# Optimization experiments

Measured on AMD Instinct MI355X. Metric: run time of the kernel, lower is better.

Reference implementation:

```python
import jax, jax.numpy as jnp
import numpy as np

EMBED, HEADS, LEVELS, POINTS, MLP = 256, 8, 3, 4, 4
SHAPES = [(60, 80), (30, 40), (15, 20)]  # (H, W) per level


def layer_norm(x, g, b):
    m = jnp.mean(x, -1, keepdims=True)
    v = jnp.mean((x - m) ** 2, -1, keepdims=True)
    return (x - m) * jax.lax.rsqrt(v + 1e-5) * g + b


def _bilinear(v, H, W, gx, gy):
    # v: [B,h,H*W,dh]; gx,gy: [B,h,Nq,P] absolute pixel coords (grid_sample align_corners=False, zero padding)
    x0 = jnp.floor(gx); y0 = jnp.floor(gy)
    wx = gx - x0; wy = gy - y0

    def g(xi, yi):
        valid = ((xi >= 0) & (xi < W) & (yi >= 0) & (yi < H)).astype(v.dtype)
        idx = jnp.clip(yi, 0, H - 1) * W + jnp.clip(xi, 0, W - 1)
        B, h, Nq, P = idx.shape
        out = jnp.take_along_axis(v, idx.reshape(B, h, Nq * P)[..., None], axis=2)
        return out.reshape(B, h, Nq, P, -1) * valid[..., None]

    x0i = x0.astype(jnp.int32); y0i = y0.astype(jnp.int32)
    return (g(x0i, y0i) * ((1 - wx) * (1 - wy))[..., None]
            + g(x0i + 1, y0i) * (wx * (1 - wy))[..., None]
            + g(x0i, y0i + 1) * ((1 - wx) * wy)[..., None]
            + g(x0i + 1, y0i + 1) * (wx * wy)[..., None])


def setup_inputs() -> dict:
    key = jax.random.key(0)
    ks = jax.random.split(key, 16)
    B, Nq, C = 2, 8192, EMBED
    Nv = sum(h * w for h, w in SHAPES)
    s = 0.02
    d = {
        'query': jax.random.normal(ks[0], (B, Nq, C), jnp.float32),
        'value': jax.random.normal(ks[1], (B, Nv, C), jnp.float32),
        'query_pos': jax.random.normal(ks[2], (B, Nq, C), jnp.float32),
        'ref_pts': jax.random.uniform(ks[3], (B, Nq, LEVELS, 2), jnp.float32),
        'spatial_shapes': jnp.array(SHAPES, jnp.int32),
        'level_start_index': jnp.array(np.cumsum([0] + [h * w for h, w in SHAPES[:-1]]), jnp.int32),
        'g1': jnp.ones((C,), jnp.float32), 'b1': jnp.zeros((C,), jnp.float32),
        'Wo': s * jax.random.normal(ks[4], (C, HEADS * LEVELS * POINTS * 2), jnp.float32),
        'bo': jnp.zeros((HEADS * LEVELS * POINTS * 2,), jnp.float32),
        'Wa': s * jax.random.normal(ks[5], (C, HEADS * LEVELS * POINTS), jnp.float32),
        'ba': jnp.zeros((HEADS * LEVELS * POINTS,), jnp.float32),
        'Wv': s * jax.random.normal(ks[6], (C, C), jnp.float32), 'bv': jnp.zeros((C,), jnp.float32),
        'Wp': s * jax.random.normal(ks[7], (C, C), jnp.float32), 'bp': jnp.zeros((C,), jnp.float32),
        'g2': jnp.ones((C,), jnp.float32), 'b2': jnp.zeros((C,), jnp.float32),
        'Wf1': s * jax.random.normal(ks[8], (C, MLP * C), jnp.float32), 'bf1': jnp.zeros((MLP * C,), jnp.float32),
        'Wf2': s * jax.random.normal(ks[9], (MLP * C, C), jnp.float32), 'bf2': jnp.zeros((C,), jnp.float32),
    }
    return d


def reference(query, value, query_pos, ref_pts, spatial_shapes, level_start_index,
              g1, b1, Wo, bo, Wa, ba, Wv, bv, Wp, bp, g2, b2, Wf1, bf1, Wf2, bf2):
    B, Nq, C = query.shape
    dh = C // HEADS
    shapes = np.asarray(spatial_shapes).tolist()
    starts = np.asarray(level_start_index).tolist()

    qn = layer_norm(query, g1, b1)           # pre-norm
    qa = qn + query_pos                       # positional embedding inside attn
    offs = (qa @ Wo + bo).reshape(B, Nq, HEADS, LEVELS, POINTS, 2)
    aw = jax.nn.softmax((qa @ Wa + ba).reshape(B, Nq, HEADS, LEVELS * POINTS), -1)
    aw = aw.reshape(B, Nq, HEADS, LEVELS, POINTS)
    v = (value @ Wv + bv).reshape(B, -1, HEADS, dh).transpose(0, 2, 1, 3)  # [B,h,Nv,dh]

    # offset_normalizer = (W, H) per level
    norm = jnp.array([[w, h] for h, w in shapes], jnp.float32)
    loc = ref_pts[:, :, None, :, None, :] + offs / norm[None, None, None, :, None, :]

    out = jnp.zeros((B, Nq, HEADS, dh), query.dtype)
    for l, (H, W) in enumerate(shapes):
        vl = jax.lax.dynamic_slice_in_dim(v, starts[l], H * W, axis=2)
        gl = loc[:, :, :, l].transpose(0, 2, 1, 3, 4)   # [B,h,Nq,P,2]
        gx = gl[..., 0] * W - 0.5
        gy = gl[..., 1] * H - 0.5
        sampled = _bilinear(vl, H, W, gx, gy)            # [B,h,Nq,P,dh]
        out = out + jnp.einsum('bhqpd,bqhp->bqhd', sampled, aw[:, :, :, l])

    attn = out.reshape(B, Nq, C) @ Wp + bp + qn          # output proj + mmcv internal residual (identity=norm1(query))
    q = query + attn                                     # layer residual
    q2 = layer_norm(q, g2, b2)
    return q + (jax.nn.gelu(q2 @ Wf1 + bf1, approximate=False) @ Wf2 + bf2)
```

## Files before the change

### kernel.cpp

```cpp
#include <hip/hip_runtime.h>
#include <math.h>


typedef short short8 __attribute__((ext_vector_type(8)));
typedef short s16x4 __attribute__((ext_vector_type(4)));
typedef __bf16 bf16x8 __attribute__((ext_vector_type(8)));
typedef float f32x4 __attribute__((ext_vector_type(4)));

__device__ __forceinline__ short f2b(float f) {
  unsigned u = __builtin_bit_cast(unsigned, f);
  u += 0x7fffu + ((u >> 16) & 1u);
  return (short)(u >> 16);
}
__device__ __forceinline__ float b2f(short s) {
  unsigned u = ((unsigned)(unsigned short)s) << 16;
  return __builtin_bit_cast(float, u);
}
__device__ __forceinline__ void b8f(short8 s, float* f) {
  const uint4 u = __builtin_bit_cast(uint4, s);
  f[0] = __builtin_bit_cast(float, u.x << 16);
  f[1] = __builtin_bit_cast(float, u.x & 0xffff0000u);
  f[2] = __builtin_bit_cast(float, u.y << 16);
  f[3] = __builtin_bit_cast(float, u.y & 0xffff0000u);
  f[4] = __builtin_bit_cast(float, u.z << 16);
  f[5] = __builtin_bit_cast(float, u.z & 0xffff0000u);
  f[6] = __builtin_bit_cast(float, u.w << 16);
  f[7] = __builtin_bit_cast(float, u.w & 0xffff0000u);
}

__device__ __forceinline__ f32x4 mfma16(short8 a, short8 b, f32x4 c) {
  return __builtin_amdgcn_mfma_f32_16x16x32_bf16(
      __builtin_bit_cast(bf16x8, a), __builtin_bit_cast(bf16x8, b), c, 0, 0, 0);
}

typedef __attribute__((address_space(3))) unsigned int lds_u32;
typedef const __attribute__((address_space(1))) unsigned int glb_u32;
__device__ __forceinline__ void glds16(const void* g, void* l) {
  __builtin_amdgcn_global_load_lds((glb_u32*)g, (lds_u32*)l, 16, 0, 0);
}

__device__ __forceinline__ float gelu1(float v) {
  return 0.5f * v * (1.f + erff(v * 0.70710678118654752f));
}

template <int EPI>
__device__ __forceinline__ void gemm64_core(
    int bx, int by,
    const short* __restrict__ A, const short* __restrict__ Bt,
    const float* __restrict__ bias, const float* __restrict__ bias2,
    void* __restrict__ Cout, int M, int Nreal, int ldc, int K, char* smem)
{
  short* sA = (short*)smem;
  short* sB = sA + 4096;
  float* sf = (float*)smem;

  const int t = threadIdx.x;
  const int wave = t >> 6, lane = t & 63;
  const int quad = lane >> 4, l16 = lane & 15;
  const int wm = (wave & 1) * 32, wn = (wave >> 1) * 64;
  const int m0 = by * 64, n0 = bx * 128;

  f32x4 acc[2][4];
#pragma unroll
  for (int i = 0; i < 2; i++)
#pragma unroll
    for (int j = 0; j < 4; j++) acc[i][j] = (f32x4){0.f, 0.f, 0.f, 0.f};

  const int srow = lane >> 3, pos = lane & 7;
  const int chunk = (pos + srow) & 7;
  const short* gA = A + (size_t)(m0 + wave * 16 + srow) * K + chunk * 8;
  const short* gB = Bt + (size_t)(n0 + wave * 32 + srow) * K + chunk * 8;

  const int nk = K >> 6;
  for (int kt = 0; kt < nk; ++kt) {
    if (kt) __syncthreads();
    const int ko = kt * 64;
#pragma unroll
    for (int g = 0; g < 2; ++g)
      glds16(gA + ko + (size_t)(g * 8) * K, sA + (wave * 16 + g * 8) * 64);
#pragma unroll
    for (int g = 0; g < 4; ++g)
      glds16(gB + ko + (size_t)(g * 8) * K, sB + (wave * 32 + g * 8) * 64);
    __syncthreads();
#pragma unroll
    for (int kk = 0; kk < 2; ++kk) {
      short8 af[2], bf[4];
      const int c = kk * 4 + quad;
#pragma unroll
      for (int i = 0; i < 2; i++) {
        const int lrA = wm + i * 16 + l16;
        af[i] = *(const short8*)&sA[lrA * 64 + ((c - lrA) & 7) * 8];
      }
#pragma unroll
      for (int j = 0; j < 4; j++) {
        const int lrB = wn + j * 16 + l16;
        bf[j] = *(const short8*)&sB[lrB * 64 + ((c - lrB) & 7) * 8];
      }
#pragma unroll
      for (int i = 0; i < 2; i++)
#pragma unroll
        for (int j = 0; j < 4; j++) acc[i][j] = mfma16(bf[j], af[i], acc[i][j]);
    }
  }
  __syncthreads();

#pragma unroll
  for (int b = 0; b < 2; ++b) {
    if (wm == b * 32) {
#pragma unroll
      for (int i = 0; i < 2; ++i) {
        const int rr = i * 16 + l16;
#pragma unroll
        for (int j = 0; j < 4; ++j)
          *(f32x4*)&sf[rr * 132 + wn + quad * 4 + j * 16] = acc[i][j];
      }
    }
    __syncthreads();
#pragma unroll
    for (int r2 = 0; r2 < 4; ++r2) {
      const int fidx = r2 * 1024 + t * 4;
      const int row = fidx >> 7, col = fidx & 127;
      const int gm = m0 + b * 32 + row;
      const int cc = n0 + col;
      if (gm < M && cc < Nreal) {
        const float4 v = *(const float4*)&sf[row * 132 + col];
        float4 bb;
        if (EPI == 4) bb = (cc < 192) ? *(const float4*)(bias + cc)
                                      : *(const float4*)(bias2 + cc - 192);
        else bb = *(const float4*)(bias + cc);
        float v0 = v.x + bb.x, v1 = v.y + bb.y, v2 = v.z + bb.z, v3 = v.w + bb.w;
        s16x4 o; o.x = f2b(v0); o.y = f2b(v1); o.z = f2b(v2); o.w = f2b(v3);
        *(s16x4*)((short*)Cout + (size_t)gm * ldc + cc) = o;
      }
    }
    __syncthreads();
  }
}

__global__ __launch_bounds__(256) void gemm_oa_v(
    const short* __restrict__ qa, const short* __restrict__ wt_oa,
    const float* __restrict__ bo, const float* __restrict__ ba,
    short* __restrict__ oabuf,
    const short* __restrict__ valbf, const short* __restrict__ wt_v,
    const float* __restrict__ bv, short* __restrict__ vproj)
{
  __shared__ __align__(16) char smem[24576];
  const int idx = blockIdx.x;
  if (idx < 768) {
    gemm64_core<4>(idx % 3, idx / 3, qa, wt_oa, bo, ba,
                   oabuf, 16384, 288, 288, 256, smem);
  } else {
    const int r = idx - 768;
    gemm64_core<5>(r % 2, r / 2, valbf, wt_v, bv, nullptr,
                   vproj, 12600, 256, 256, 256, smem);
  }
}

__global__ __launch_bounds__(1024, 4) void wp_mlp(
    const short* __restrict__ sampled,
    const short* __restrict__ wtp,
    const float* __restrict__ bp,
    const short* __restrict__ qnb,
    const float* __restrict__ query,
    const float* __restrict__ g2, const float* __restrict__ b2v,
    const short* __restrict__ wf1,
    const float* __restrict__ b1v,
    const short* __restrict__ wf2,
    const float* __restrict__ bf2v,
    float* __restrict__ outp)
{
  __shared__ __align__(16) char smem[163840];
  float* Q  = (float*)smem;
  short* H  = (short*)(smem + 65536);
  float* QY = (float*)(smem + 65536);
  short* RA = (short*)(smem + 131072);

  const int t = threadIdx.x;
  const int w = t >> 6, lane = t & 63;
  const int quad = lane >> 4, l16 = lane & 15;
  const int wm2 = w >> 3, wn8 = w & 7;
  const int m0 = blockIdx.x * 64;

#pragma unroll
  for (int q = 0; q < 2; ++q) {
    const int row = q * 32 + w * 2 + (lane >> 5);
    const int pos = lane & 31;
    const int cl = (pos & ~7) | ((pos + row) & 7);
    glds16(sampled + (size_t)(m0 + row) * 256 + cl * 8, RA + q * 8192 + w * 512);
  }
#pragma unroll
  for (int q = 0; q < 4; ++q) {
    const int row = q * 16 + w;
    glds16(query + (size_t)(m0 + row) * 256 + lane * 4, QY + row * 256);
  }
  __syncthreads();

  {
    f32x4 accp[2][2];
#pragma unroll
    for (int i = 0; i < 2; i++)
#pragma unroll
      for (int j = 0; j < 2; j++) accp[i][j] = (f32x4){0.f, 0.f, 0.f, 0.f};
#pragma unroll
    for (int kk = 0; kk < 8; ++kk) {
      const int c = kk * 4 + quad;
      short8 bfr[2], afr[2];
#pragma unroll
      for (int j = 0; j < 2; ++j) {
        const int n1 = wn8 * 2 + j;
        bfr[j] = *(const short8*)(wtp + ((size_t)n1 * 32 + c) * 128 + l16 * 8);
      }
#pragma unroll
      for (int i = 0; i < 2; ++i) {
        const int r = wm2 * 32 + i * 16 + l16;
        const int pos = (c & ~7) | ((c - r) & 7);
        afr[i] = *(const short8*)(RA + r * 256 + pos * 8);
      }
#pragma unroll
      for (int i = 0; i < 2; ++i)
#pragma unroll
        for (int j = 0; j < 2; ++j) accp[i][j] = mfma16(bfr[j], afr[i], accp[i][j]);
    }
#pragma unroll
    for (int i = 0; i < 2; ++i)
#pragma unroll
      for (int j = 0; j < 2; ++j) {
        const int r = wm2 * 32 + i * 16 + l16;
        const int c = wn8 * 32 + j * 16 + quad * 4;
        *(f32x4*)&Q[r * 256 + (c ^ ((r & 7) << 2))] = accp[i][j];
      }
  }
  __syncthreads();

  {
    const float4 bbp  = *(const float4*)(bp + lane * 4);
    const float4 gv   = *(const float4*)(g2 + lane * 4);
    const float4 bb2  = *(const float4*)(b2v + lane * 4);
#pragma unroll
    for (int rep = 0; rep < 4; ++rep) {
      const int row = rep * 16 + w;
      const int gm = m0 + row;
      const int cs = (lane * 4) ^ ((row & 7) << 2);
      const float4 a  = *(const float4*)&Q[row * 256 + cs];
      const float4 qv = *(const float4*)&QY[row * 256 + lane * 4];
      const s16x4 qn  = *(const s16x4*)(qnb + (size_t)gm * 256 + lane * 4);
      float v0 = a.x + bbp.x + b2f(qn.x) + qv.x;
      float v1 = a.y + bbp.y + b2f(qn.y) + qv.y;
      float v2 = a.z + bbp.z + b2f(qn.z) + qv.z;
      float v3 = a.w + bbp.w + b2f(qn.w) + qv.w;
      float s = v0 + v1 + v2 + v3;
#pragma unroll
      for (int o = 32; o; o >>= 1) s += __shfl_xor(s, o);
      const float mean = s * (1.f / 256.f);
      const float d0 = v0 - mean, d1 = v1 - mean, d2 = v2 - mean, d3 = v3 - mean;
      float ss = d0 * d0 + d1 * d1 + d2 * d2 + d3 * d3;
#pragma unroll
      for (int o = 32; o; o >>= 1) ss += __shfl_xor(ss, o);
      const float inv = rsqrtf(ss * (1.f / 256.f) + 1e-5f);
      *(f32x4*)&Q[row * 256 + cs] = (f32x4){v0, v1, v2, v3};
      const int col = lane * 4;
      const int c = col >> 3;
      const int pos = (c & ~7) | ((c - row) & 7);
      s16x4 o2;
      o2.x = f2b(d0 * inv * gv.x + bb2.x);
      o2.y = f2b(d1 * inv * gv.y + bb2.y);
      o2.z = f2b(d2 * inv * gv.z + bb2.z);
      o2.w = f2b(d3 * inv * gv.w + bb2.w);
      *(s16x4*)(RA + row * 256 + pos * 8 + (col & 7)) = o2;
    }
  }
  __syncthreads();

  f32x4 acc2[2][2];
#pragma unroll
  for (int i = 0; i < 2; i++)
#pragma unroll
    for (int j = 0; j < 2; j++) acc2[i][j] = (f32x4){0.f, 0.f, 0.f, 0.f};

  for (int h = 0; h < 2; ++h) {
    if (h) __syncthreads();
    f32x4 acc[4][2];
#pragma unroll
    for (int i = 0; i < 4; i++)
#pragma unroll
      for (int j = 0; j < 2; j++) acc[i][j] = (f32x4){0.f, 0.f, 0.f, 0.f};
#pragma unroll
    for (int kk = 0; kk < 8; ++kk) {
      const int cg = kk * 4 + quad;
      short8 bfr[2], afr[4];
#pragma unroll
      for (int j = 0; j < 2; ++j) {
        const int n1 = h * 32 + w * 2 + j;
        bfr[j] = *(const short8*)(wf1 + ((size_t)n1 * 32 + cg) * 128 + l16 * 8);
      }
#pragma unroll
      for (int i = 0; i < 4; ++i) {
        const int r = i * 16 + l16;
        const int pos = (cg & ~7) | ((cg - r) & 7);
        afr[i] = *(const short8*)(RA + r * 256 + pos * 8);
      }
#pragma unroll
      for (int i = 0; i < 4; ++i)
#pragma unroll
        for (int j = 0; j < 2; ++j) acc[i][j] = mfma16(bfr[j], afr[i], acc[i][j]);
    }
#pragma unroll
    for (int j = 0; j < 2; ++j) {
      const int coll = (w * 2 + j) * 16 + quad * 4;
      const float4 bb = *(const float4*)(b1v + h * 512 + coll);
      const int c = coll >> 3;
#pragma unroll
      for (int i = 0; i < 4; ++i) {
        const int r = i * 16 + l16;
        const int pos = (c & ~7) | ((c - r) & 7);
        s16x4 o;
        o.x = f2b(gelu1(acc[i][j].x + bb.x));
        o.y = f2b(gelu1(acc[i][j].y + bb.y));
        o.z = f2b(gelu1(acc[i][j].z + bb.z));
        o.w = f2b(gelu1(acc[i][j].w + bb.w));
        *(s16x4*)(H + r * 512 + pos * 8 + (coll & 7)) = o;
      }
    }
    __syncthreads();

#pragma unroll 4
    for (int kk = 0; kk < 16; ++kk) {
      const int cl = kk * 4 + quad;
      short8 bfr[2], afr[2];
#pragma unroll
      for (int j = 0; j < 2; ++j) {
        const int n1 = wn8 * 2 + j;
        bfr[j] = *(const short8*)(wf2 + ((size_t)n1 * 128 + h * 64 + cl) * 128 + l16 * 8);
      }
#pragma unroll
      for (int i = 0; i < 2; ++i) {
        const int r = wm2 * 32 + i * 16 + l16;
        const int pos = (cl & ~7) | ((cl - r) & 7);
        afr[i] = *(const short8*)(H + r * 512 + pos * 8);
      }
#pragma unroll
      for (int i = 0; i < 2; ++i)
#pragma unroll
        for (int j = 0; j < 2; ++j) acc2[i][j] = mfma16(bfr[j], afr[i], acc2[i][j]);
    }
  }
  __syncthreads();

#pragma unroll
  for (int i = 0; i < 2; ++i)
#pragma unroll
    for (int j = 0; j < 2; ++j) {
      const int r = wm2 * 32 + i * 16 + l16;
      const int c = wn8 * 32 + j * 16 + quad * 4;
      *(f32x4*)&QY[r * 256 + (c ^ ((r & 7) << 2))] = acc2[i][j];
    }
  __syncthreads();

  {
    const float4 bbf = *(const float4*)(bf2v + lane * 4);
#pragma unroll
    for (int rep = 0; rep < 4; ++rep) {
      const int row = rep * 16 + w;
      const int gm = m0 + row;
      const int cs = (lane * 4) ^ ((row & 7) << 2);
      const float4 v  = *(const float4*)&QY[row * 256 + cs];
      const float4 qb = *(const float4*)&Q[row * 256 + cs];
      *(float4*)(outp + (size_t)gm * 256 + lane * 4) =
          make_float4(v.x + bbf.x + qb.x, v.y + bbf.y + qb.y,
                      v.z + bbf.z + qb.z, v.w + bbf.w + qb.w);
    }
  }
}

__global__ __launch_bounds__(256) void prep_all(
    const float* __restrict__ Wo, const float* __restrict__ Wa,
    const float* __restrict__ Wv, const float* __restrict__ Wp,
    const float* __restrict__ Wf1, const float* __restrict__ Wf2,
    short* __restrict__ t_oa, short* __restrict__ t_v, short* __restrict__ t_p,
    short* __restrict__ t_f1, short* __restrict__ t_f2,
    const float* __restrict__ value, short* __restrict__ valbf,
    const float* __restrict__ query, const float* __restrict__ query_pos,
    const float* __restrict__ g1, const float* __restrict__ b1,
    short* __restrict__ qnb, short* __restrict__ qa)
{
  __shared__ float tile[32][33];
  const int t = threadIdx.x;
  const int blk = blockIdx.x;

  if (blk < 1792) {
    const int bxa = blk & 255, bya = blk >> 8;
    int K, N, noff; const float* src; short* dst;
    switch (bya) {
      case 0: src = Wo;      dst = t_oa; K = 256;  N = 192;  noff = 0;   break;
      case 1: src = Wa;      dst = t_oa; K = 256;  N = 96;   noff = 192; break;
      case 2: src = nullptr; dst = t_oa; K = 256;  N = 96;   noff = 288; break;
      case 3: src = Wv;      dst = t_v;  K = 256;  N = 256;  noff = 0;   break;
      case 4: src = Wp;      dst = t_p;  K = 256;  N = 256;  noff = 0;   break;
      case 5: src = Wf1;     dst = t_f1; K = 256;  N = 1024; noff = 0;   break;
      default: src = Wf2;    dst = t_f2; K = 1024; N = 256;  noff = 0;   break;
    }
    const bool fragpack = (bya >= 4);
    const int tilesK = K >> 5;
    const int nt = tilesK * (N >> 5);
    if (bxa >= nt) return;
    const int tk = bxa % tilesK, tn = bxa / tilesK;
    const int k0 = tk * 32, n0 = tn * 32;
    const int r = t >> 3, c4 = (t & 7) * 4;
    float4 v = make_float4(0.f, 0.f, 0.f, 0.f);
    if (src) v = *(const float4*)(src + (size_t)(k0 + r) * N + n0 + c4);
    tile[r][c4] = v.x; tile[r][c4 + 1] = v.y; tile[r][c4 + 2] = v.z; tile[r][c4 + 3] = v.w;
    __syncthreads();
    const int nn = t >> 3, kc = (t & 7) * 4;
    s16x4 o;
    o.x = f2b(tile[kc][nn]); o.y = f2b(tile[kc + 1][nn]);
    o.z = f2b(tile[kc + 2][nn]); o.w = f2b(tile[kc + 3][nn]);
    if (fragpack) {
      const int n = n0 + nn, k = k0 + kc;
      *(s16x4*)(dst + ((size_t)(n >> 4) * (K >> 3) + (k >> 3)) * 128 +
                (n & 15) * 8 + (k & 7)) = o;
    } else {
      *(s16x4*)(dst + (size_t)(noff + n0 + nn) * K + k0 + kc) = o;
    }
  } else if (blk < 1792 + 3169) {
    const int i = ((blk - 1792) * 256 + t) * 4;
    if (i >= 12672 * 256) return;
    s16x4 o = (s16x4){0, 0, 0, 0};
    if (i < 12600 * 256) {
      float4 v = *(const float4*)(value + i);
      o.x = f2b(v.x); o.y = f2b(v.y); o.z = f2b(v.z); o.w = f2b(v.w);
    }
    *(s16x4*)(valbf + i) = o;
  } else {
    const int row  = (blk - 4961) * 4 + (t >> 6);
    const int lane = t & 63;
    const float4 v = ((const float4*)(query + (size_t)row * 256))[lane];
    float s = v.x + v.y + v.z + v.w;
#pragma unroll
    for (int o = 32; o; o >>= 1) s += __shfl_xor(s, o);
    const float mean = s * (1.f / 256.f);
    const float dx = v.x - mean, dy = v.y - mean, dz = v.z - mean, dw = v.w - mean;
    float s2 = dx * dx + dy * dy + dz * dz + dw * dw;
#pragma unroll
    for (int o = 32; o; o >>= 1) s2 += __shfl_xor(s2, o);
    const float inv = rsqrtf(s2 * (1.f / 256.f) + 1e-5f);
    const float4 gv = ((const float4*)g1)[lane];
    const float4 bv = ((const float4*)b1)[lane];
    const float4 o1 = make_float4(dx * inv * gv.x + bv.x, dy * inv * gv.y + bv.y,
                                  dz * inv * gv.z + bv.z, dw * inv * gv.w + bv.w);
    s16x4 ob; ob.x = f2b(o1.x); ob.y = f2b(o1.y); ob.z = f2b(o1.z); ob.w = f2b(o1.w);
    ((s16x4*)(qnb + (size_t)row * 256))[lane] = ob;
    const float4 pv = ((const float4*)(query_pos + (size_t)row * 256))[lane];
    s16x4 op;
    op.x = f2b(o1.x + pv.x); op.y = f2b(o1.y + pv.y);
    op.z = f2b(o1.z + pv.z); op.w = f2b(o1.w + pv.w);
    ((s16x4*)(qa + (size_t)row * 256))[lane] = op;
  }
}

__global__ __launch_bounds__(256) void deform_fused(
    const short* __restrict__ vproj, const short* __restrict__ oa,
    const float* __restrict__ refp, short* __restrict__ out)
{
  __shared__ int4 sIdx[768];
  __shared__ s16x4 sW[768];
  const int t = threadIdx.x;

  if (t < 64) {
    const int row = blockIdx.x * 8 + (t >> 3), h = t & 7;
    const short* oarow = oa + (size_t)row * 288;
    float off[24];
    {
      const short8* op = (const short8*)(oarow + h * 24);
      b8f(op[0], off); b8f(op[1], off + 8); b8f(op[2], off + 16);
    }
    float lg[12];
    {
      const s16x4* ap = (const s16x4*)(oarow + 192 + h * 12);
#pragma unroll
      for (int i = 0; i < 3; i++) {
        const s16x4 v = ap[i];
        lg[i * 4] = b2f(v.x); lg[i * 4 + 1] = b2f(v.y);
        lg[i * 4 + 2] = b2f(v.z); lg[i * 4 + 3] = b2f(v.w);
      }
    }
    const float* rp = refp + (size_t)row * 6;
    const float Rx[3] = {rp[0], rp[2], rp[4]}, Ry[3] = {rp[1], rp[3], rp[5]};
    float mx = lg[0];
#pragma unroll
    for (int i = 1; i < 12; i++) mx = fmaxf(mx, lg[i]);
    float sum = 0.f;
#pragma unroll
    for (int i = 0; i < 12; i++) { lg[i] = __expf(lg[i] - mx); sum += lg[i]; }
    const float inv = 1.f / sum;
    const int b = row >> 13;
    const int Hs[3] = {60, 30, 15}, Ws[3] = {80, 40, 20}, St[3] = {0, 4800, 6000};
#pragma unroll
    for (int p = 0; p < 12; p++) {
      const int l = p >> 2;
      const int W = Ws[l], H = Hs[l];
      const float gx = Rx[l] * W + off[p * 2]     - 0.5f;
      const float gy = Ry[l] * H + off[p * 2 + 1] - 0.5f;
      const float x0f = floorf(gx), y0f = floorf(gy);
      const float wx = gx - x0f, wy = gy - y0f;
      const int x0 = (int)x0f, y0 = (int)y0f;
      const float aw = lg[p] * inv;
      float cw[4] = {(1.f - wx) * (1.f - wy), wx * (1.f - wy),
                     (1.f - wx) * wy, wx * wy};
      const int base = b * 6300 + St[l];
      int ci[4];
#pragma unroll
      for (int k = 0; k < 4; k++) {
        const int xx = x0 + (k & 1), yy = y0 + (k >> 1);
        const bool valid = (xx >= 0) & (xx < W) & (yy >= 0) & (yy < H);
        const int xc = min(max(xx, 0), W - 1);
        const int yc = min(max(yy, 0), H - 1);
        ci[k] = ((base + yc * W + xc) << 8) + h * 32;
        cw[k] = valid ? cw[k] * aw : 0.f;
      }
      sIdx[t * 12 + p] = make_int4(ci[0], ci[1], ci[2], ci[3]);
      s16x4 wv; wv.x = f2b(cw[0]); wv.y = f2b(cw[1]); wv.z = f2b(cw[2]); wv.w = f2b(cw[3]);
      sW[t * 12 + p] = wv;
    }
  }
  __syncthreads();

  const int lu = t >> 2, c4 = (t & 3) * 8;
  float acc[8];
#pragma unroll
  for (int i = 0; i < 8; i++) acc[i] = 0.f;
#pragma unroll 2
  for (int p = 0; p < 12; p++) {
    const int4 idx = sIdx[lu * 12 + p];
    const s16x4 wb = sW[lu * 12 + p];
    const float w0 = b2f(wb.x), w1 = b2f(wb.y), w2 = b2f(wb.z), w3 = b2f(wb.w);
    const short8 v0 = *(const short8*)(vproj + idx.x + c4);
    const short8 v1 = *(const short8*)(vproj + idx.y + c4);
    const short8 v2 = *(const short8*)(vproj + idx.z + c4);
    const short8 v3 = *(const short8*)(vproj + idx.w + c4);
    float f0[8], f1[8], f2[8], f3[8];
    b8f(v0, f0); b8f(v1, f1); b8f(v2, f2); b8f(v3, f3);
#pragma unroll
    for (int j = 0; j < 8; j++)
      acc[j] += w0 * f0[j] + w1 * f1[j] + w2 * f2[j] + w3 * f3[j];
  }
  short8 o;
#pragma unroll
  for (int j = 0; j < 8; j++) o[j] = f2b(acc[j]);
  *(short8*)(out + (size_t)(blockIdx.x * 256 + t) * 8) = o;
}

extern "C" void kernel_launch(void* const* d_in, const int* in_sizes, int n_in,
                              void* d_out, int out_size, void* d_ws, size_t ws_size,
                              hipStream_t stream)
{
  const float* query     = (const float*)d_in[0];
  const float* value     = (const float*)d_in[1];
  const float* query_pos = (const float*)d_in[2];
  const float* ref_pts   = (const float*)d_in[3];
  const float* g1  = (const float*)d_in[6];
  const float* b1  = (const float*)d_in[7];
  const float* Wo  = (const float*)d_in[8];
  const float* bo  = (const float*)d_in[9];
  const float* Wa  = (const float*)d_in[10];
  const float* ba  = (const float*)d_in[11];
  const float* Wv  = (const float*)d_in[12];
  const float* bv  = (const float*)d_in[13];
  const float* Wp  = (const float*)d_in[14];
  const float* bp  = (const float*)d_in[15];
  const float* g2  = (const float*)d_in[16];
  const float* b2  = (const float*)d_in[17];
  const float* Wf1 = (const float*)d_in[18];
  const float* bf1 = (const float*)d_in[19];
  const float* Wf2 = (const float*)d_in[20];
  const float* bf2 = (const float*)d_in[21];

  char* ws = (char*)d_ws;
  short* wt_oa   = (short*)(ws + 0);
  short* wt_v    = (short*)(ws + 196608);
  short* wt_p    = (short*)(ws + 327680);
  short* wt_f1   = (short*)(ws + 458752);
  short* wt_f2   = (short*)(ws + 983040);
  short* qnb     = (short*)(ws + 1507328);
  short* qa      = (short*)(ws + 18284544);
  short* oabuf   = (short*)(ws + 26673152);
  short* vproj   = (short*)(ws + 45547520);
  short* sampled = (short*)(ws + 51998720);
  short* valbf   = (short*)(ws + 77164544);
  float* outp = (float*)d_out;

  prep_all<<<9057, 256, 0, stream>>>(Wo, Wa, Wv, Wp, Wf1, Wf2,
                                     wt_oa, wt_v, wt_p, wt_f1, wt_f2,
                                     value, valbf, query, query_pos,
                                     g1, b1, qnb, qa);
  gemm_oa_v<<<1162, 256, 0, stream>>>(qa, wt_oa, bo, ba, oabuf,
                                      valbf, wt_v, bv, vproj);
  deform_fused<<<2048, 256, 0, stream>>>(vproj, oabuf, ref_pts, sampled);
  wp_mlp<<<256, 1024, 0, stream>>>(sampled, wt_p, bp, qnb, query, g2, b2,
                                   wt_f1, bf1, wt_f2, bf2, outp);
}
```

Measured before the change: 214.8 us.

## Shrink wp_mlp row tile to 32 rows with 512-thread blocks

The fused output-projection/MLP kernel now processes 32 rows per block with 8 waves instead of 64 rows with 16 waves. The grid doubles to 512 blocks and LDS per block halves, which spreads work across more CUs than the previous 256 blocks. Each wave now owns one 16-row slice and a wider column strip, reusing one A fragment across 4 to 8 B fragments. A VGPR cap of 128 is added via an attribute. The cost is that each weight fragment is fetched for half as many rows, so global weight traffic roughly doubles, and the register cap risks spills with 8 accumulators.

After: 248.8 us. +15.8%, slower.

```diff
diff --git a/kernel.cpp b/kernel.cpp
--- a/kernel.cpp
+++ b/kernel.cpp
@@ -6,6 +6,16 @@
 typedef short s16x4 __attribute__((ext_vector_type(4)));
 typedef __bf16 bf16x8 __attribute__((ext_vector_type(8)));
 typedef float f32x4 __attribute__((ext_vector_type(4)));
+
+#if defined(__has_attribute)
+#if __has_attribute(amdgpu_num_vgpr)
+#define WPMLP_REGS __attribute__((amdgpu_num_vgpr(128)))
+#else
+#define WPMLP_REGS
+#endif
+#else
+#define WPMLP_REGS
+#endif
 
 __device__ __forceinline__ short f2b(float f) {
   unsigned u = __builtin_bit_cast(unsigned, f);
@@ -156,7 +166,7 @@
   }
 }
 
-__global__ __launch_bounds__(1024, 4) void wp_mlp(
+__global__ __launch_bounds__(512) WPMLP_REGS void wp_mlp(
     const short* __restrict__ sampled,
     const short* __restrict__ wtp,
     const float* __restrict__ bp,
@@ -169,66 +179,59 @@
     const float* __restrict__ bf2v,
     float* __restrict__ outp)
 {
-  __shared__ __align__(16) char smem[163840];
+  __shared__ __align__(16) char smem[81920];
   float* Q  = (float*)smem;
-  short* H  = (short*)(smem + 65536);
-  float* QY = (float*)(smem + 65536);
-  short* RA = (short*)(smem + 131072);
+  short* H  = (short*)(smem + 32768);
+  float* QY = (float*)(smem + 32768);
+  short* RA = (short*)(smem + 65536);
 
   const int t = threadIdx.x;
   const int w = t >> 6, lane = t & 63;
   const int quad = lane >> 4, l16 = lane & 15;
-  const int wm2 = w >> 3, wn8 = w & 7;
-  const int m0 = blockIdx.x * 64;
+  const int wm2 = w >> 2, wn4 = w & 3;
+  const int m0 = blockIdx.x * 32;
 
 #pragma unroll
   for (int q = 0; q < 2; ++q) {
-    const int row = q * 32 + w * 2 + (lane >> 5);
-    const int pos = lane & 31;
-    const int cl = (pos & ~7) | ((pos + row) & 7);
-    glds16(sampled + (size_t)(m0 + row) * 256 + cl * 8, RA + q * 8192 + w * 512);
+    const int g = q * 512 + t;
+    const int row = g >> 5, p = g & 31;
+    const int cl = (p & ~7) | ((p + row) & 7);
+    glds16(sampled + (size_t)(m0 + row) * 256 + cl * 8,
+           RA + (q * 512 + w * 64) * 8);
   }
 #pragma unroll
   for (int q = 0; q < 4; ++q) {
-    const int row = q * 16 + w;
-    glds16(query + (size_t)(m0 + row) * 256 + lane * 4, QY + row * 256);
+    const int g = q * 512 + t;
+    glds16(query + (size_t)(m0 + (g >> 6)) * 256 + (g & 63) * 4,
+           QY + (q * 512 + w * 64) * 4);
   }
   __syncthreads();
 
   {
-    f32x4 accp[2][2];
-#pragma unroll
-    for (int i = 0; i < 2; i++)
-#pragma unroll
-      for (int j = 0; j < 2; j++) accp[i][j] = (f32x4){0.f, 0.f, 0.f, 0.f};
+    f32x4 accp[4];
+#pragma unroll
+    for (int j = 0; j < 4; j++) accp[j] = (f32x4){0.f, 0.f, 0.f, 0.f};
 #pragma unroll
     for (int kk = 0; kk < 8; ++kk) {
       const int c = kk * 4 + quad;
-      short8 bfr[2], afr[2];
-#pragma unroll
-      for (int j = 0; j < 2; ++j) {
-        const int n1 = wn8 * 2 + j;
+      const int r = wm2 * 16 + l16;
+      const int pos = (c & ~7) | ((c - r) & 7);
+      const short8 afr = *(const short8*)(RA + r * 256 + pos * 8);
+      short8 bfr[4];
+#pragma unroll
+      for (int j = 0; j < 4; ++j) {
+        const int n1 = wn4 * 4 + j;
         bfr[j] = *(const short8*)(wtp + ((size_t)n1 * 32 + c) * 128 + l16 * 8);
       }
 #pragma unroll
-      for (int i = 0; i < 2; ++i) {
-        const int r = wm2 * 32 + i * 16 + l16;
-        const int pos = (c & ~7) | ((c - r) & 7);
-        afr[i] = *(const short8*)(RA + r * 256 + pos * 8);
-      }
-#pragma unroll
-      for (int i = 0; i < 2; ++i)
-#pragma unroll
-        for (int j = 0; j < 2; ++j) accp[i][j] = mfma16(bfr[j], afr[i], accp[i][j]);
-    }
-#pragma unroll
-    for (int i = 0; i < 2; ++i)
-#pragma unroll
-      for (int j = 0; j < 2; ++j) {
-        const int r = wm2 * 32 + i * 16 + l16;
-        const int c = wn8 * 32 + j * 16 + quad * 4;
-        *(f32x4*)&Q[r * 256 + (c ^ ((r & 7) << 2))] = accp[i][j];
-      }
+      for (int j = 0; j < 4; ++j) accp[j] = mfma16(bfr[j], afr, accp[j]);
+    }
+#pragma unroll
+    for (int j = 0; j < 4; ++j) {
+      const int r = wm2 * 16 + l16;
+      const int c = wn4 * 64 + j * 16 + quad * 4;
+      *(f32x4*)&Q[r * 256 + (c ^ ((r & 7) << 2))] = accp[j];
+    }
   }
   __syncthreads();
 
@@ -238,7 +241,7 @@
     const float4 bb2  = *(const float4*)(b2v + lane * 4);
 #pragma unroll
     for (int rep = 0; rep < 4; ++rep) {
-      const int row = rep * 16 + w;
+      const int row = rep * 8 + w;
       const int gm = m0 + row;
       const int cs = (lane * 4) ^ ((row & 7) << 2);
       const float4 a  = *(const float4*)&Q[row * 256 + cs];
@@ -271,96 +274,77 @@
   }
   __syncthreads();
 
-  f32x4 acc2[2][2];
-#pragma unroll
-  for (int i = 0; i < 2; i++)
-#pragma unroll
-    for (int j = 0; j < 2; j++) acc2[i][j] = (f32x4){0.f, 0.f, 0.f, 0.f};
+  f32x4 acc2[4];
+#pragma unroll
+  for (int j = 0; j < 4; j++) acc2[j] = (f32x4){0.f, 0.f, 0.f, 0.f};
 
   for (int h = 0; h < 2; ++h) {
     if (h) __syncthreads();
-    f32x4 acc[4][2];
-#pragma unroll
-    for (int i = 0; i < 4; i++)
-#pragma unroll
-      for (int j = 0; j < 2; j++) acc[i][j] = (f32x4){0.f, 0.f, 0.f, 0.f};
+    f32x4 acc1[8];
+#pragma unroll
+    for (int j = 0; j < 8; j++) acc1[j] = (f32x4){0.f, 0.f, 0.f, 0.f};
 #pragma unroll
     for (int kk = 0; kk < 8; ++kk) {
       const int cg = kk * 4 + quad;
-      short8 bfr[2], afr[4];
-#pragma unroll
-      for (int j = 0; j < 2; ++j) {
-        const int n1 = h * 32 + w * 2 + j;
+      const int r = wm2 * 16 + l16;
+      const int pos = (cg & ~7) | ((cg - r) & 7);
+      const short8 afr = *(const short8*)(RA + r * 256 + pos * 8);
+      short8 bfr[8];
+#pragma unroll
+      for (int j = 0; j < 8; ++j) {
+        const int n1 = h * 32 + wn4 * 8 + j;
         bfr[j] = *(const short8*)(wf1 + ((size_t)n1 * 32 + cg) * 128 + l16 * 8);
       }
 #pragma unroll
-      for (int i = 0; i < 4; ++i) {
-        const int r = i * 16 + l16;
-        const int pos = (cg & ~7) | ((cg - r) & 7);
-        afr[i] = *(const short8*)(RA + r * 256 + pos * 8);
-      }
-#pragma unroll
-      for (int i = 0; i < 4; ++i)
-#pragma unroll
-        for (int j = 0; j < 2; ++j) acc[i][j] = mfma16(bfr[j], afr[i], acc[i][j]);
-    }
-#pragma unroll
-    for (int j = 0; j < 2; ++j) {
-      const int coll = (w * 2 + j) * 16 + quad * 4;
+      for (int j = 0; j < 8; ++j) acc1[j] = mfma16(bfr[j], afr, acc1[j]);
+    }
+#pragma unroll
+    for (int j = 0; j < 8; ++j) {
+      const int coll = wn4 * 128 + j * 16 + quad * 4;
       const float4 bb = *(const float4*)(b1v + h * 512 + coll);
       const int c = coll >> 3;
-#pragma unroll
-      for (int i = 0; i < 4; ++i) {
-        const int r = i * 16 + l16;
-        const int pos = (c & ~7) | ((c - r) & 7);
-        s16x4 o;
-        o.x = f2b(gelu1(acc[i][j].x + bb.x));
-        o.y = f2b(gelu1(acc[i][j].y + bb.y));
-        o.z = f2b(gelu1(acc[i][j].z + bb.z));
-        o.w = f2b(gelu1(acc[i][j].w + bb.w));
-        *(s16x4*)(H + r * 512 + pos * 8 + (coll & 7)) = o;
-      }
+      const int r = wm2 * 16 + l16;
+      const int pos = (c & ~7) | ((c - r) & 7);
+      s16x4 o;
+      o.x = f2b(gelu1(acc1[j].x + bb.x));
+      o.y = f2b(gelu1(acc1[j].y + bb.y));
+      o.z = f2b(gelu1(acc1[j].z + bb.z));
+      o.w = f2b(gelu1(acc1[j].w + bb.w));
+      *(s16x4*)(H + r * 512 + pos * 8 + (coll & 7)) = o;
     }
     __syncthreads();
 
 #pragma unroll 4
     for (int kk = 0; kk < 16; ++kk) {
       const int cl = kk * 4 + quad;
-      short8 bfr[2], afr[2];
-#pragma unroll
-      for (int j = 0; j < 2; ++j) {
-        const int n1 = wn8 * 2 + j;
+      const int r = wm2 * 16 + l16;
+      const int pos = (cl & ~7) | ((cl - r) & 7);
+      const short8 afr = *(const short8*)(H + r * 512 + pos * 8);
+      short8 bfr[4];
+#pragma unroll
+      for (int j = 0; j < 4; ++j) {
+        const int n1 = wn4 * 4 + j;
         bfr[j] = *(const short8*)(wf2 + ((size_t)n1 * 128 + h * 64 + cl) * 128 + l16 * 8);
       }
 #pragma unroll
-      for (int i = 0; i < 2; ++i) {
-        const int r = wm2 * 32 + i * 16 + l16;
-        const int pos = (cl & ~7) | ((cl - r) & 7);
-        afr[i] = *(const short8*)(H + r * 512 + pos * 8);
-      }
-#pragma unroll
-      for (int i = 0; i < 2; ++i)
-#pragma unroll
-        for (int j = 0; j < 2; ++j) acc2[i][j] = mfma16(bfr[j], afr[i], acc2[i][j]);
-    }
-  }
-  __syncthreads();
-
-#pragma unroll
-  for (int i = 0; i < 2; ++i)
-#pragma unroll
-    for (int j = 0; j < 2; ++j) {
-      const int r = wm2 * 32 + i * 16 + l16;
-      const int c = wn8 * 32 + j * 16 + quad * 4;
-      *(f32x4*)&QY[r * 256 + (c ^ ((r & 7) << 2))] = acc2[i][j];
-    }
+      for (int j = 0; j < 4; ++j) acc2[j] = mfma16(bfr[j], afr, acc2[j]);
+    }
+  }
+  __syncthreads();
+
+#pragma unroll
+  for (int j = 0; j < 4; ++j) {
+    const int r = wm2 * 16 + l16;
+    const int c = wn4 * 64 + j * 16 + quad * 4;
+    *(f32x4*)&QY[r * 256 + (c ^ ((r & 7) << 2))] = acc2[j];
+  }
   __syncthreads();
 
   {
     const float4 bbf = *(const float4*)(bf2v + lane * 4);
 #pragma unroll
     for (int rep = 0; rep < 4; ++rep) {
-      const int row = rep * 16 + w;
+      const int row = rep * 8 + w;
       const int gm = m0 + row;
       const int cs = (lane * 4) ^ ((row & 7) << 2);
       const float4 v  = *(const float4*)&QY[row * 256 + cs];
@@ -595,6 +579,6 @@
   gemm_oa_v<<<1162, 256, 0, stream>>>(qa, wt_oa, bo, ba, oabuf,
                                       valbf, wt_v, bv, vproj);
   deform_fused<<<2048, 256, 0, stream>>>(vproj, oabuf, ref_pts, sampled);
-  wp_mlp<<<256, 1024, 0, stream>>>(sampled, wt_p, bp, qnb, query, g2, b2,
-                                   wt_f1, bf1, wt_f2, bf2, outp);
-}
+  wp_mlp<<<512, 512, 0, stream>>>(sampled, wt_p, bp, qnb, query, g2, b2,
+                                  wt_f1, bf1, wt_f2, bf2, outp);
+}
```

## Restructure wp_mlp hidden loop into four 256-wide chunks and shrink LDS

Applied to the files above, without the earlier changes.

The fused projection+MLP kernel now processes the 1024-wide hidden layer in four 256-column chunks instead of two 512-wide halves. Both GEMMs use the same 2x8 wave tiling, which shrinks the H buffer and total LDS from 160KB to 128KB. The query residual is read directly from global memory instead of being staged in LDS, and the final bias+residual is fused into Q in registers before the store. The launch bound no longer requests a minimum of 4 waves per EU and caps VGPRs at 128. In exchange there are more block-wide barriers per row tile and the weight fragments are reloaded per chunk.

Result: faster. 206.9 us (-3.6%).

```diff
diff --git a/kernel.cpp b/kernel.cpp
--- a/kernel.cpp
+++ b/kernel.cpp
@@ -6,6 +6,16 @@
 typedef short s16x4 __attribute__((ext_vector_type(4)));
 typedef __bf16 bf16x8 __attribute__((ext_vector_type(8)));
 typedef float f32x4 __attribute__((ext_vector_type(4)));
+
+#if defined(__has_attribute)
+#if __has_attribute(amdgpu_num_vgpr)
+#define WPMLP_REGS __attribute__((amdgpu_num_vgpr(128)))
+#else
+#define WPMLP_REGS
+#endif
+#else
+#define WPMLP_REGS
+#endif
 
 __device__ __forceinline__ short f2b(float f) {
   unsigned u = __builtin_bit_cast(unsigned, f);
@@ -156,7 +166,7 @@
   }
 }
 
-__global__ __launch_bounds__(1024, 4) void wp_mlp(
+__global__ __launch_bounds__(1024) WPMLP_REGS void wp_mlp(
     const short* __restrict__ sampled,
     const short* __restrict__ wtp,
     const float* __restrict__ bp,
@@ -169,11 +179,10 @@
     const float* __restrict__ bf2v,
     float* __restrict__ outp)
 {
-  __shared__ __align__(16) char smem[163840];
+  __shared__ __align__(16) char smem[131072];
   float* Q  = (float*)smem;
   short* H  = (short*)(smem + 65536);
-  float* QY = (float*)(smem + 65536);
-  short* RA = (short*)(smem + 131072);
+  short* RA = (short*)(smem + 98304);
 
   const int t = threadIdx.x;
   const int w = t >> 6, lane = t & 63;
@@ -182,16 +191,12 @@
   const int m0 = blockIdx.x * 64;
 
 #pragma unroll
-  for (int q = 0; q < 2; ++q) {
-    const int row = q * 32 + w * 2 + (lane >> 5);
-    const int pos = lane & 31;
-    const int cl = (pos & ~7) | ((pos + row) & 7);
-    glds16(sampled + (size_t)(m0 + row) * 256 + cl * 8, RA + q * 8192 + w * 512);
-  }
-#pragma unroll
-  for (int q = 0; q < 4; ++q) {
-    const int row = q * 16 + w;
-    glds16(query + (size_t)(m0 + row) * 256 + lane * 4, QY + row * 256);
+  for (int qq = 0; qq < 2; ++qq) {
+    const int g = qq * 1024 + t;
+    const int row = g >> 5, p = g & 31;
+    const int cl = (p & ~7) | ((p + row) & 7);
+    glds16(sampled + (size_t)(m0 + row) * 256 + cl * 8,
+           RA + (qq * 1024 + w * 64) * 8);
   }
   __syncthreads();
 
@@ -204,12 +209,7 @@
 #pragma unroll
     for (int kk = 0; kk < 8; ++kk) {
       const int c = kk * 4 + quad;
-      short8 bfr[2], afr[2];
-#pragma unroll
-      for (int j = 0; j < 2; ++j) {
-        const int n1 = wn8 * 2 + j;
-        bfr[j] = *(const short8*)(wtp + ((size_t)n1 * 32 + c) * 128 + l16 * 8);
-      }
+      short8 afr[2], bfr[2];
 #pragma unroll
       for (int i = 0; i < 2; ++i) {
         const int r = wm2 * 32 + i * 16 + l16;
@@ -217,6 +217,11 @@
         afr[i] = *(const short8*)(RA + r * 256 + pos * 8);
       }
 #pragma unroll
+      for (int j = 0; j < 2; ++j) {
+        const int n1 = wn8 * 2 + j;
+        bfr[j] = *(const short8*)(wtp + ((size_t)n1 * 32 + c) * 128 + l16 * 8);
+      }
+#pragma unroll
       for (int i = 0; i < 2; ++i)
 #pragma unroll
         for (int j = 0; j < 2; ++j) accp[i][j] = mfma16(bfr[j], afr[i], accp[i][j]);
@@ -226,8 +231,8 @@
 #pragma unroll
       for (int j = 0; j < 2; ++j) {
         const int r = wm2 * 32 + i * 16 + l16;
-        const int c = wn8 * 32 + j * 16 + quad * 4;
-        *(f32x4*)&Q[r * 256 + (c ^ ((r & 7) << 2))] = accp[i][j];
+        const int cc = wn8 * 32 + j * 16 + quad * 4;
+        *(f32x4*)&Q[r * 256 + (cc ^ ((r & 7) << 2))] = accp[i][j];
       }
   }
   __syncthreads();
@@ -242,7 +247,7 @@
       const int gm = m0 + row;
       const int cs = (lane * 4) ^ ((row & 7) << 2);
       const float4 a  = *(const float4*)&Q[row * 256 + cs];
-      const float4 qv = *(const float4*)&QY[row * 256 + lane * 4];
+      const float4 qv = *(const float4*)(query + (size_t)gm * 256 + lane * 4);
       const s16x4 qn  = *(const s16x4*)(qnb + (size_t)gm * 256 + lane * 4);
       float v0 = a.x + bbp.x + b2f(qn.x) + qv.x;
       float v1 = a.y + bbp.y + b2f(qn.y) + qv.y;
@@ -277,66 +282,66 @@
 #pragma unroll
     for (int j = 0; j < 2; j++) acc2[i][j] = (f32x4){0.f, 0.f, 0.f, 0.f};
 
-  for (int h = 0; h < 2; ++h) {
-    if (h) __syncthreads();
-    f32x4 acc[4][2];
-#pragma unroll
-    for (int i = 0; i < 4; i++)
-#pragma unroll
-      for (int j = 0; j < 2; j++) acc[i][j] = (f32x4){0.f, 0.f, 0.f, 0.f};
+  for (int q = 0; q < 4; ++q) {
+    if (q) __syncthreads();
+    f32x4 acc1[2][2];
+#pragma unroll
+    for (int i = 0; i < 2; i++)
+#pragma unroll
+      for (int j = 0; j < 2; j++) acc1[i][j] = (f32x4){0.f, 0.f, 0.f, 0.f};
 #pragma unroll
     for (int kk = 0; kk < 8; ++kk) {
       const int cg = kk * 4 + quad;
-      short8 bfr[2], afr[4];
-#pragma unroll
-      for (int j = 0; j < 2; ++j) {
-        const int n1 = h * 32 + w * 2 + j;
-        bfr[j] = *(const short8*)(wf1 + ((size_t)n1 * 32 + cg) * 128 + l16 * 8);
-      }
-#pragma unroll
-      for (int i = 0; i < 4; ++i) {
-        const int r = i * 16 + l16;
+      short8 afr[2], bfr[2];
+#pragma unroll
+      for (int i = 0; i < 2; ++i) {
+        const int r = wm2 * 32 + i * 16 + l16;
         const int pos = (cg & ~7) | ((cg - r) & 7);
         afr[i] = *(const short8*)(RA + r * 256 + pos * 8);
       }
 #pragma unroll
-      for (int i = 0; i < 4; ++i)
-#pragma unroll
-        for (int j = 0; j < 2; ++j) acc[i][j] = mfma16(bfr[j], afr[i], acc[i][j]);
+      for (int j = 0; j < 2; ++j) {
+        const int n1 = q * 16 + wn8 * 2 + j;
+        bfr[j] = *(const short8*)(wf1 + ((size_t)n1 * 32 + cg) * 128 + l16 * 8);
+      }
+#pragma unroll
+      for (int i = 0; i < 2; ++i)
+#pragma unroll
+        for (int j = 0; j < 2; ++j) acc1[i][j] = mfma16(bfr[j], afr[i], acc1[i][j]);
     }
 #pragma unroll
     for (int j = 0; j < 2; ++j) {
-      const int coll = (w * 2 + j) * 16 + quad * 4;
-      const float4 bb = *(const float4*)(b1v + h * 512 + coll);
+      const int coll = wn8 * 32 + j * 16 + quad * 4;
+      const float4 bb = *(const float4*)(b1v + q * 256 + coll);
       const int c = coll >> 3;
 #pragma unroll
-      for (int i = 0; i < 4; ++i) {
-        const int r = i * 16 + l16;
+      for (int i = 0; i < 2; ++i) {
+        const int r = wm2 * 32 + i * 16 + l16;
         const int pos = (c & ~7) | ((c - r) & 7);
         s16x4 o;
-        o.x = f2b(gelu1(acc[i][j].x + bb.x));
-        o.y = f2b(gelu1(acc[i][j].y + bb.y));
-        o.z = f2b(gelu1(acc[i][j].z + bb.z));
-        o.w = f2b(gelu1(acc[i][j].w + bb.w));
-        *(s16x4*)(H + r * 512 + pos * 8 + (coll & 7)) = o;
+        o.x = f2b(gelu1(acc1[i][j].x + bb.x));
+        o.y = f2b(gelu1(acc1[i][j].y + bb.y));
+        o.z = f2b(gelu1(acc1[i][j].z + bb.z));
+        o.w = f2b(gelu1(acc1[i][j].w + bb.w));
+        *(s16x4*)(H + r * 256 + pos * 8 + (coll & 7)) = o;
       }
     }
     __syncthreads();
 
 #pragma unroll 4
-    for (int kk = 0; kk < 16; ++kk) {
+    for (int kk = 0; kk < 8; ++kk) {
       const int cl = kk * 4 + quad;
-      short8 bfr[2], afr[2];
-#pragma unroll
-      for (int j = 0; j < 2; ++j) {
-        const int n1 = wn8 * 2 + j;
-        bfr[j] = *(const short8*)(wf2 + ((size_t)n1 * 128 + h * 64 + cl) * 128 + l16 * 8);
-      }
+      short8 afr[2], bfr[2];
 #pragma unroll
       for (int i = 0; i < 2; ++i) {
         const int r = wm2 * 32 + i * 16 + l16;
         const int pos = (cl & ~7) | ((cl - r) & 7);
-        afr[i] = *(const short8*)(H + r * 512 + pos * 8);
+        afr[i] = *(const short8*)(H + r * 256 + pos * 8);
+      }
+#pragma unroll
+      for (int j = 0; j < 2; ++j) {
+        const int n1 = wn8 * 2 + j;
+        bfr[j] = *(const short8*)(wf2 + ((size_t)n1 * 128 + q * 32 + cl) * 128 + l16 * 8);
       }
 #pragma unroll
       for (int i = 0; i < 2; ++i)
@@ -344,31 +349,31 @@
         for (int j = 0; j < 2; ++j) acc2[i][j] = mfma16(bfr[j], afr[i], acc2[i][j]);
     }
   }
+
+  {
+#pragma unroll
+    for (int i = 0; i < 2; ++i)
+#pragma unroll
+      for (int j = 0; j < 2; ++j) {
+        const int r = wm2 * 32 + i * 16 + l16;
+        const int cc = wn8 * 32 + j * 16 + quad * 4;
+        const int cs = cc ^ ((r & 7) << 2);
+        const float4 bb = *(const float4*)(bf2v + cc);
+        const float4 qb = *(const float4*)&Q[r * 256 + cs];
+        *(f32x4*)&Q[r * 256 + cs] =
+            (f32x4){qb.x + acc2[i][j].x + bb.x, qb.y + acc2[i][j].y + bb.y,
+                    qb.z + acc2[i][j].z + bb.z, qb.w + acc2[i][j].w + bb.w};
+      }
+  }
   __syncthreads();
 
 #pragma unroll
-  for (int i = 0; i < 2; ++i)
-#pragma unroll
-    for (int j = 0; j < 2; ++j) {
-      const int r = wm2 * 32 + i * 16 + l16;
-      const int c = wn8 * 32 + j * 16 + quad * 4;
-      *(f32x4*)&QY[r * 256 + (c ^ ((r & 7) << 2))] = acc2[i][j];
-    }
-  __syncthreads();
-
-  {
-    const float4 bbf = *(const float4*)(bf2v + lane * 4);
-#pragma unroll
-    for (int rep = 0; rep < 4; ++rep) {
-      const int row = rep * 16 + w;
-      const int gm = m0 + row;
-      const int cs = (lane * 4) ^ ((row & 7) << 2);
-      const float4 v  = *(const float4*)&QY[row * 256 + cs];
-      const float4 qb = *(const float4*)&Q[row * 256 + cs];
-      *(float4*)(outp + (size_t)gm * 256 + lane * 4) =
-          make_float4(v.x + bbf.x + qb.x, v.y + bbf.y + qb.y,
-                      v.z + bbf.z + qb.z, v.w + bbf.w + qb.w);
-    }
+  for (int rep = 0; rep < 4; ++rep) {
+    const int row = rep * 16 + w;
+    const int gm = m0 + row;
+    const int cs = (lane * 4) ^ ((row & 7) << 2);
+    const float4 v = *(const float4*)&Q[row * 256 + cs];
+    *(float4*)(outp + (size_t)gm * 256 + lane * 4) = v;
   }
 }
 
```
